# Kernel optimization log

Measured on AMD Instinct MI355X. Metric: run time of the kernel, lower is better.

## Reference

```python
import jax, jax.numpy as jnp
import numpy as np

B, N, D = 4, 4096, 1024
H, F = 16, 256
HD = D // H
EPS_ATTN = 1e-8
EPS_LN = 1e-5


def setup_inputs() -> dict:
    key = jax.random.key(0)
    ks = jax.random.split(key, 10)
    def kaiming(k, shape):
        fan_in = shape[1]
        return jax.random.normal(k, shape, jnp.float32) * jnp.sqrt(2.0 / fan_in)
    # orthogonal-ish random projection (plain gaussian init, then QR per head)
    pm = jax.random.normal(ks[0], (H, HD, F), jnp.float32)
    return {
        "x": jax.random.normal(ks[1], (B, N, D), jnp.float32),
        "proj": pm,
        "w_qkv": kaiming(ks[2], (3 * D, D)),
        "w_out": kaiming(ks[3], (D, D)),
        "b_out": jnp.zeros((D,), jnp.float32),
        "gamma": jnp.ones((D,), jnp.float32),
        "beta": jnp.zeros((D,), jnp.float32),
        "w1": kaiming(ks[4], (4 * D, D)),
        "b1": jnp.zeros((4 * D,), jnp.float32),
        "w2": kaiming(ks[5], (D, 4 * D)),
        "b2": jnp.zeros((D,), jnp.float32),
    }


def _layernorm(x, gamma, beta):
    mu = jnp.mean(x, axis=-1, keepdims=True)
    var = jnp.var(x, axis=-1, keepdims=True)
    return (x - mu) * jax.lax.rsqrt(var + EPS_LN) * gamma + beta


def reference(x, proj, w_qkv, w_out, b_out, gamma, beta, w1, b1, w2, b2):
    residual = x
    b, n, d = x.shape
    qkv = x @ w_qkv.T                      # (b,n,3d)
    q, k, v = jnp.split(qkv, 3, axis=-1)
    def to_heads(t):
        return t.reshape(b, n, H, HD).transpose(0, 2, 1, 3)  # (b,h,n,hd)
    q, k, v = to_heads(q), to_heads(k), to_heads(v)
    # kernel feature maps: elu(x)+1
    q_f = jax.nn.elu(jnp.einsum('bhnd,hdf->bhnf', q, proj)) + 1.0
    k_f = jax.nn.elu(jnp.einsum('bhnd,hdf->bhnf', k, proj)) + 1.0
    # non-causal FAVOR+ linear attention
    kv = jnp.einsum('bhnf,bhnd->bhfd', k_f, v)               # (b,h,f,hd)
    attn = jnp.einsum('bhnf,bhfd->bhnd', q_f, kv)            # (b,h,n,hd)
    k_sum = jnp.sum(k_f, axis=2)                             # (b,h,f)
    z = 1.0 / (jnp.einsum('bhnf,bhf->bhn', q_f, k_sum) + EPS_ATTN)
    attn = attn * z[..., None]
    attn = attn.transpose(0, 2, 1, 3).reshape(b, n, d)
    x = residual + attn @ w_out.T + b_out
    x = _layernorm(x, gamma, beta)
    h = jax.nn.gelu(x @ w1.T + b1, approximate=False)
    x = x + h @ w2.T + b2
    x = _layernorm(x, gamma, beta)
    return x
```

## Files before the change

kernel.cpp:

```cpp
#include <hip/hip_runtime.h>
#include <math.h>

typedef unsigned short u16;
typedef __bf16 bf16x8 __attribute__((ext_vector_type(8)));
typedef float f32x4 __attribute__((ext_vector_type(4)));
typedef unsigned short u16x4 __attribute__((ext_vector_type(4)));
typedef unsigned short u16x8 __attribute__((ext_vector_type(8)));

#define DEV static __device__ __forceinline__

DEV float bf2f(u16 u) { union { unsigned int i; float f; } x; x.i = ((unsigned int)u) << 16; return x.f; }
DEV u16 f2bf(float f) { union { float f; unsigned int i; } x; x.f = f; unsigned int r = x.i + 0x7fffu + ((x.i >> 16) & 1u); return (u16)(r >> 16); }

DEV void load_lds16(const void* g, void* l) {
  __builtin_amdgcn_global_load_lds((__attribute__((address_space(1))) void*)g,
                                   (__attribute__((address_space(3))) void*)l, 16, 0, 0);
}

#define MMAQ(AREG, BREG, MH, NH)                                                            \
  do {                                                                                      \
    __builtin_amdgcn_s_setprio(1);                                                          \
    _Pragma("unroll") for (int m_ = 0; m_ < 4; ++m_)                                        \
      _Pragma("unroll") for (int n_ = 0; n_ < 2; ++n_)                                      \
        _Pragma("unroll") for (int kk_ = 0; kk_ < 2; ++kk_)                                 \
          acc[(MH)*4 + m_][(NH)*2 + n_] = __builtin_amdgcn_mfma_f32_16x16x32_bf16(          \
              AREG[m_][kk_], BREG[n_][kk_], acc[(MH)*4 + m_][(NH)*2 + n_], 0, 0, 0);        \
    __builtin_amdgcn_s_setprio(0);                                                          \
  } while (0)

template<int EPI>
__global__ __launch_bounds__(512, 1)
void gemm256(const u16* __restrict__ A, const u16* __restrict__ B, void* __restrict__ Cv,
             const float* __restrict__ aux0, const float* __restrict__ aux1,
             int M, int N, int K, int lda, int ldb, int ldc)
{
  __shared__ __align__(16) unsigned char smem[131072];
  const int tid = threadIdx.x;
  int bx = blockIdx.x, by = blockIdx.y;
  {
    int nwg = gridDim.x * gridDim.y;
    if ((nwg & 7) == 0) {
      int wg = by * gridDim.x + bx;
      int swz = (wg & 7) * (nwg >> 3) + (wg >> 3);
      bx = swz % gridDim.x; by = swz / gridDim.x;
    }
  }
  const int m0 = by * 256, n0 = bx * 256;
  const int wid = tid >> 6, lane = tid & 63;
  const int wr = wid >> 2, wc = wid & 3;
  const int ln15 = lane & 15, lq = lane >> 4;
  const int bhalf = wc >> 1;
  const int sRow = tid >> 3, sCh = tid & 7;

  f32x4 acc[8][4] = {};
  bf16x8 aR[4][2], b0R[2][2], b1R[2][2];

  auto stageHalf = [&](const u16* G, int ld, int grs, int k0, int ldsoff) {
#pragma unroll
    for (int i = 0; i < 2; ++i) {
      int row = i * 64 + sRow;
      const unsigned char* src = (const unsigned char*)(G + (size_t)(grs + row) * ld + k0)
                               + ((sCh ^ (row & 7)) << 4);
      load_lds16(src, smem + ldsoff + row * 128 + sCh * 16);
    }
  };
  auto stageTile = [&](int k0, int dbuf) {
    stageHalf(A, lda, m0,       k0, (dbuf * 2 + 0) * 16384);
    stageHalf(A, lda, m0 + 128, k0, (dbuf * 2 + 1) * 16384);
    stageHalf(B, ldb, n0,       k0, 65536 + (dbuf * 2 + 0) * 16384);
    stageHalf(B, ldb, n0 + 128, k0, 65536 + (dbuf * 2 + 1) * 16384);
  };
  auto loadA = [&](int cur, int mh) {
    const unsigned char* base = smem + (cur * 2 + wr) * 16384;
#pragma unroll
    for (int m = 0; m < 4; ++m) {
      int rl = (mh * 4 + m) * 16 + ln15;
#pragma unroll
      for (int kk = 0; kk < 2; ++kk)
        aR[m][kk] = *(const bf16x8*)(base + rl * 128 + (((kk * 4 + lq) ^ (rl & 7)) << 4));
    }
  };
  auto loadB = [&](int cur, int nh, bf16x8 (&bq)[2][2]) {
    const unsigned char* base = smem + 65536 + (cur * 2 + bhalf) * 16384;
#pragma unroll
    for (int n = 0; n < 2; ++n) {
      int rb = (wc & 1) * 64 + (nh * 2 + n) * 16 + ln15;
#pragma unroll
      for (int kk = 0; kk < 2; ++kk)
        bq[n][kk] = *(const bf16x8*)(base + rb * 128 + (((kk * 4 + lq) ^ (rb & 7)) << 4));
    }
  };

  const int nkt = K >> 6;

  stageTile(0, 0);
  asm volatile("s_waitcnt vmcnt(0)" ::: "memory");
  __builtin_amdgcn_s_barrier();

  for (int t = 0; t < nkt; ++t) {
    const int cur = t & 1;
    const bool pf = (t + 1 < nkt);
    loadA(cur, 0);
    loadB(cur, 0, b0R);
    if (pf) stageTile((t + 1) << 6, cur ^ 1);
    __builtin_amdgcn_s_barrier();
    MMAQ(aR, b0R, 0, 0);
    __builtin_amdgcn_s_barrier();
    loadB(cur, 1, b1R);
    __builtin_amdgcn_s_barrier();
    MMAQ(aR, b1R, 0, 1);
    __builtin_amdgcn_s_barrier();
    loadA(cur, 1);
    __builtin_amdgcn_s_barrier();
    MMAQ(aR, b0R, 1, 0);
    __builtin_amdgcn_s_barrier();
    MMAQ(aR, b1R, 1, 1);
    if (pf) { asm volatile("s_waitcnt vmcnt(0)" ::: "memory"); }
    __builtin_amdgcn_s_barrier();
  }

#pragma unroll
  for (int m = 0; m < 8; ++m) {
#pragma unroll
    for (int n = 0; n < 4; ++n) {
      int col = n0 + wc * 64 + n * 16 + ln15;
#pragma unroll
      for (int j = 0; j < 4; ++j) {
        int row = m0 + wr * 128 + m * 16 + lq * 4 + j;
        float v = acc[m][n][j];
        size_t idx = (size_t)row * ldc + col;
        if (EPI == 0) {
          ((u16*)Cv)[idx] = f2bf(v);
        } else if (EPI == 3) {
          ((float*)Cv)[idx] = v + aux0[col] + aux1[idx];
        } else if (EPI == 4) {
          float g = v + aux0[col];
          float o = 0.5f * g * (1.f + erff(g * 0.70710678118f));
          ((u16*)Cv)[idx] = f2bf(o);
        }
      }
    }
  }
}

__global__ __launch_bounds__(256, 2)
void fused_kv(const u16* __restrict__ qkv, const u16* __restrict__ projT,
              float* __restrict__ kvpart, float* __restrict__ ksumpart)
{
  __shared__ __align__(16) unsigned char ktS[2][8192];
  __shared__ __align__(16) unsigned char vtS[2][8192];
  __shared__ __align__(16) unsigned char kfS[32768];
  const int tid = threadIdx.x;
  const int bh = blockIdx.y, chunk = blockIdx.x;
  const int b = bh >> 4, h = bh & 15;
  const int wid = tid >> 6, lane = tid & 63;
  const int ln15 = lane & 15, lq = lane >> 4;
  const int vN = tid >> 2, vD = (tid & 3) * 16;
  const int vCn = vN >> 3, vWb = (vN & 7) * 2;

  bf16x8 pf[4][2];
#pragma unroll
  for (int m = 0; m < 4; ++m)
#pragma unroll
    for (int kk = 0; kk < 2; ++kk) {
      int f = wid * 64 + m * 16 + ln15;
      pf[m][kk] = *(const bf16x8*)(projT + (size_t)h * 16384 + (size_t)f * 64 + (kk * 4 + lq) * 8);
    }

  float ksum_r = 0.f;
  f32x4 acc2[4][4] = {};
  const int nbase = chunk * 512;

  {
    const u16* kg = qkv + ((size_t)b * 4096 + nbase) * 3072 + 1024 + h * 64;
#pragma unroll
    for (int i = 0; i < 2; ++i) {
      int c = i * 256 + tid; int r = c >> 3, ch = c & 7;
      load_lds16((const unsigned char*)(kg + (size_t)r * 3072) + ((ch ^ (r & 7)) << 4),
                 ktS[0] + r * 128 + ch * 16);
    }
    const u16* vg = qkv + ((size_t)b * 4096 + nbase + vN) * 3072 + 2048 + h * 64 + vD;
    u16x8 va = *(const u16x8*)vg;
    u16x8 vb = *(const u16x8*)(vg + 8);
#pragma unroll
    for (int j = 0; j < 8; ++j) {
      int d = vD + j;
      *(u16*)(vtS[0] + d * 128 + ((vCn ^ (d & 7)) << 4) + vWb) = va[j];
    }
#pragma unroll
    for (int j = 0; j < 8; ++j) {
      int d = vD + 8 + j;
      *(u16*)(vtS[0] + d * 128 + ((vCn ^ (d & 7)) << 4) + vWb) = vb[j];
    }
  }
  __syncthreads();

  for (int t = 0; t < 8; ++t) {
    const int cur = t & 1, nxt = cur ^ 1;
    u16x8 va, vb;
    const bool havenext = (t + 1 < 8);
    if (havenext) {
      int n1 = nbase + (t + 1) * 64;
      const u16* kg = qkv + ((size_t)b * 4096 + n1) * 3072 + 1024 + h * 64;
#pragma unroll
      for (int i = 0; i < 2; ++i) {
        int c = i * 256 + tid; int r = c >> 3, ch = c & 7;
        load_lds16((const unsigned char*)(kg + (size_t)r * 3072) + ((ch ^ (r & 7)) << 4),
                   ktS[nxt] + r * 128 + ch * 16);
      }
      const u16* vg = qkv + ((size_t)b * 4096 + n1 + vN) * 3072 + 2048 + h * 64 + vD;
      va = *(const u16x8*)vg;
      vb = *(const u16x8*)(vg + 8);
    }

    bf16x8 bvk[2][4];
#pragma unroll
    for (int kk = 0; kk < 2; ++kk)
#pragma unroll
      for (int n = 0; n < 4; ++n) {
        int r = n * 16 + ln15, kc = kk * 4 + lq;
        bvk[kk][n] = *(const bf16x8*)(ktS[cur] + r * 128 + ((kc ^ (r & 7)) << 4));
      }
#pragma unroll
    for (int m = 0; m < 4; ++m) {
      f32x4 a1[4] = {};
#pragma unroll
      for (int kk = 0; kk < 2; ++kk)
#pragma unroll
        for (int n = 0; n < 4; ++n)
          a1[n] = __builtin_amdgcn_mfma_f32_16x16x32_bf16(pf[m][kk], bvk[kk][n], a1[n], 0, 0, 0);
#pragma unroll
      for (int n = 0; n < 4; ++n) {
        int nloc = n * 16 + ln15;
        int c = nloc >> 3, wb = (nloc & 7) * 2;
#pragma unroll
        for (int j = 0; j < 4; ++j) {
          int f = wid * 64 + m * 16 + lq * 4 + j;
          float v = a1[n][j];
          float o = v > 0.f ? v + 1.f : __expf(v);
          *(u16*)(kfS + f * 128 + ((c ^ (f & 7)) << 4) + wb) = f2bf(o);
        }
      }
    }
    __syncthreads();

    {
      int f = tid;
      float s = 0.f;
#pragma unroll
      for (int c = 0; c < 8; ++c) {
        u16x8 v = *(const u16x8*)(kfS + f * 128 + ((c ^ (f & 7)) << 4));
#pragma unroll
        for (int j = 0; j < 8; ++j) s += bf2f(v[j]);
      }
      ksum_r += s;
    }
#pragma unroll
    for (int kk = 0; kk < 2; ++kk) {
      int kc = kk * 4 + lq;
      bf16x8 af[4], bv[4];
#pragma unroll
      for (int m = 0; m < 4; ++m) { int r = wid * 64 + m * 16 + ln15; af[m] = *(const bf16x8*)(kfS + r * 128 + ((kc ^ (r & 7)) << 4)); }
#pragma unroll
      for (int n = 0; n < 4; ++n) { int r = n * 16 + ln15; bv[n] = *(const bf16x8*)(vtS[cur] + r * 128 + ((kc ^ (r & 7)) << 4)); }
#pragma unroll
      for (int m = 0; m < 4; ++m)
#pragma unroll
        for (int n = 0; n < 4; ++n)
          acc2[m][n] = __builtin_amdgcn_mfma_f32_16x16x32_bf16(af[m], bv[n], acc2[m][n], 0, 0, 0);
    }
    if (havenext) {
#pragma unroll
      for (int j = 0; j < 8; ++j) {
        int d = vD + j;
        *(u16*)(vtS[nxt] + d * 128 + ((vCn ^ (d & 7)) << 4) + vWb) = va[j];
      }
#pragma unroll
      for (int j = 0; j < 8; ++j) {
        int d = vD + 8 + j;
        *(u16*)(vtS[nxt] + d * 128 + ((vCn ^ (d & 7)) << 4) + vWb) = vb[j];
      }
    }
    __syncthreads();
  }

  const size_t pbase = ((size_t)bh * 8 + chunk) * 16384;
#pragma unroll
  for (int half = 0; half < 2; ++half) {
#pragma unroll
    for (int m = 0; m < 4; ++m)
#pragma unroll
      for (int n2 = 0; n2 < 2; ++n2) {
        int n = half * 2 + n2;
        int dloc = n2 * 16 + ln15;
        int f = wid * 64 + m * 16 + lq * 4;
        *(f32x4*)(kfS + dloc * 1024 + ((f * 4) ^ ((dloc & 7) << 4))) = acc2[m][n];
      }
    __syncthreads();
#pragma unroll
    for (int k = 0; k < 8; ++k) {
      int dloc = k * 4 + wid;
      f32x4 val = *(const f32x4*)(kfS + dloc * 1024 + ((lane * 16) ^ ((dloc & 7) << 4)));
      *(f32x4*)(kvpart + pbase + (size_t)(half * 32 + dloc) * 256 + lane * 4) = val;
    }
    __syncthreads();
  }
  ksumpart[((size_t)bh * 8 + chunk) * 256 + tid] = ksum_r;
}

__global__ __launch_bounds__(256) void kv_finalize(const float* __restrict__ kvpart,
    const float* __restrict__ ksumpart, u16* __restrict__ kvT, float* __restrict__ ksum)
{
  int bx = blockIdx.x, bh = bx >> 2, dq = bx & 3, tid = threadIdx.x;
  const float* base = kvpart + (size_t)bh * 131072;
  u16* out = kvT + (size_t)bh * 16384;
#pragma unroll
  for (int k = 0; k < 16; ++k) {
    int idx = dq * 4096 + k * 256 + tid;
    float s = 0.f;
#pragma unroll
    for (int c = 0; c < 8; ++c) s += base[(size_t)c * 16384 + idx];
    out[idx] = f2bf(s);
  }
  if (dq == 0) {
    float s = 0.f;
#pragma unroll
    for (int c = 0; c < 8; ++c) s += ksumpart[((size_t)bh * 8 + c) * 256 + tid];
    ksum[(size_t)bh * 256 + tid] = s;
  }
}

__global__ __launch_bounds__(256, 3)
void fused_attn(const u16* __restrict__ qkv, const u16* __restrict__ projT,
                const u16* __restrict__ kvT, const float* __restrict__ ksum,
                u16* __restrict__ attnb)
{
  __shared__ __align__(16) unsigned char qtS[8192];
  __shared__ __align__(16) unsigned char qfS[32768];
  __shared__ float zpart[64][4];
  __shared__ float zS[64];
  const int tid = threadIdx.x;
  const int bh = blockIdx.y, nt = blockIdx.x;
  const int b = bh >> 4, h = bh & 15;
  const int wid = tid >> 6, lane = tid & 63;
  const int ln15 = lane & 15, lq = lane >> 4;
  const int n0 = nt * 64;

  bf16x8 pf[4][2];
#pragma unroll
  for (int n = 0; n < 4; ++n)
#pragma unroll
    for (int kk = 0; kk < 2; ++kk) {
      int f = wid * 64 + n * 16 + ln15;
      pf[n][kk] = *(const bf16x8*)(projT + (size_t)h * 16384 + (size_t)f * 64 + (kk * 4 + lq) * 8);
    }

  const u16* qg = qkv + ((size_t)b * 4096 + n0) * 3072 + h * 64;
#pragma unroll
  for (int i = 0; i < 2; ++i) {
    int c = i * 256 + tid; int r = c >> 3, ch = c & 7;
    load_lds16((const unsigned char*)(qg + (size_t)r * 3072) + ((ch ^ (r & 7)) << 4),
               qtS + r * 128 + ch * 16);
  }
  __syncthreads();

#pragma unroll
  for (int m = 0; m < 4; ++m) {
    bf16x8 af[2];
#pragma unroll
    for (int kk = 0; kk < 2; ++kk) {
      int r = m * 16 + ln15, kc = kk * 4 + lq;
      af[kk] = *(const bf16x8*)(qtS + r * 128 + ((kc ^ (r & 7)) << 4));
    }
    f32x4 a1[4] = {};
#pragma unroll
    for (int kk = 0; kk < 2; ++kk)
#pragma unroll
      for (int n = 0; n < 4; ++n)
        a1[n] = __builtin_amdgcn_mfma_f32_16x16x32_bf16(af[kk], pf[n][kk], a1[n], 0, 0, 0);
#pragma unroll
    for (int n = 0; n < 4; ++n) {
      int f = wid * 64 + n * 16 + ln15;
      int c = f >> 3, wb = (f & 7) * 2;
#pragma unroll
      for (int j = 0; j < 4; ++j) {
        int row = m * 16 + lq * 4 + j;
        float v = a1[n][j];
        float o = v > 0.f ? v + 1.f : __expf(v);
        *(u16*)(qfS + row * 512 + ((c ^ (row & 7)) << 4) + wb) = f2bf(o);
      }
    }
  }
  __syncthreads();

  {
    int n = tid & 63, q = tid >> 6;
    const float* kp = ksum + (size_t)bh * 256;
    float s = 0.f;
#pragma unroll
    for (int c = q * 8; c < q * 8 + 8; ++c) {
      u16x8 v = *(const u16x8*)(qfS + n * 512 + ((c ^ (n & 7)) << 4));
#pragma unroll
      for (int j = 0; j < 8; ++j) s += bf2f(v[j]) * kp[c * 8 + j];
    }
    zpart[n][q] = s;
  }
  __syncthreads();
  if (tid < 64) zS[tid] = 1.f / (zpart[tid][0] + zpart[tid][1] + zpart[tid][2] + zpart[tid][3] + 1e-8f);
  __syncthreads();

  f32x4 a2[4] = {};
  const u16* kvg = kvT + (size_t)bh * 16384;
#pragma unroll
  for (int kk = 0; kk < 8; ++kk) {
    int kc = kk * 4 + lq;
    int r = wid * 16 + ln15;
    bf16x8 af = *(const bf16x8*)(qfS + r * 512 + ((kc ^ (r & 7)) << 4));
#pragma unroll
    for (int nf = 0; nf < 4; ++nf) {
      int d = nf * 16 + ln15;
      bf16x8 bv = *(const bf16x8*)(kvg + (size_t)d * 256 + kc * 8);
      a2[nf] = __builtin_amdgcn_mfma_f32_16x16x32_bf16(af, bv, a2[nf], 0, 0, 0);
    }
  }
#pragma unroll
  for (int nf = 0; nf < 4; ++nf)
#pragma unroll
    for (int j = 0; j < 4; ++j) {
      int d = nf * 16 + ln15;
      int n = wid * 16 + lq * 4 + j;
      float v = a2[nf][j] * zS[n];
      attnb[((size_t)b * 4096 + n0 + n) * 1024 + h * 64 + d] = f2bf(v);
    }
}

__global__ __launch_bounds__(256) void cast_kernel(const float* __restrict__ in, u16* __restrict__ out, int n4)
{
  int i = blockIdx.x * 256 + threadIdx.x;
  if (i >= n4) return;
  float4 v = ((const float4*)in)[i];
  u16x4 o = { f2bf(v.x), f2bf(v.y), f2bf(v.z), f2bf(v.w) };
  ((u16x4*)out)[i] = o;
}

__global__ __launch_bounds__(256) void projt_kernel(const float* __restrict__ proj, u16* __restrict__ out)
{
  int i = blockIdx.x * 256 + threadIdx.x;
  int d = i & 63, f = (i >> 6) & 255, h = i >> 14;
  out[i] = f2bf(proj[((size_t)h * 64 + d) * 256 + f]);
}

__global__ __launch_bounds__(256) void ln_kernel(const float* __restrict__ in, const float* __restrict__ gamma,
                                                 const float* __restrict__ beta, float* __restrict__ outF,
                                                 u16* __restrict__ outB)
{
  int row = blockIdx.x, tid = threadIdx.x;
  float4 v = ((const float4*)(in + (size_t)row * 1024))[tid];
  float s = v.x + v.y + v.z + v.w;
  float q = v.x * v.x + v.y * v.y + v.z * v.z + v.w * v.w;
  for (int off = 32; off; off >>= 1) { s += __shfl_down(s, off); q += __shfl_down(q, off); }
  __shared__ float rs[4], rq[4];
  int wid = tid >> 6, lane = tid & 63;
  if (!lane) { rs[wid] = s; rq[wid] = q; }
  __syncthreads();
  s = rs[0] + rs[1] + rs[2] + rs[3];
  q = rq[0] + rq[1] + rq[2] + rq[3];
  float mu = s * (1.f / 1024.f);
  float rstd = rsqrtf(q * (1.f / 1024.f) - mu * mu + 1e-5f);
  float4 g = ((const float4*)gamma)[tid];
  float4 bb = ((const float4*)beta)[tid];
  float4 o;
  o.x = (v.x - mu) * rstd * g.x + bb.x;
  o.y = (v.y - mu) * rstd * g.y + bb.y;
  o.z = (v.z - mu) * rstd * g.z + bb.z;
  o.w = (v.w - mu) * rstd * g.w + bb.w;
  ((float4*)(outF + (size_t)row * 1024))[tid] = o;
  if (outB) {
    u16x4 ob = { f2bf(o.x), f2bf(o.y), f2bf(o.z), f2bf(o.w) };
    ((u16x4*)(outB + (size_t)row * 1024))[tid] = ob;
  }
}

#define O_WQKVB   0L
#define O_WOUTB   6291456L
#define O_W1B     8388608L
#define O_W2B     16777216L
#define O_PROJT   25165824L
#define O_KSUM    25690112L
#define O_KSP     26804224L
#define O_KVB     27852800L
#define O_QFG     37289984L
#define O_QKVB    70844416L
#define O_ATTNB   171507712L
#define WS_NEED   205062144L

extern "C" void kernel_launch(void* const* d_in, const int* in_sizes, int n_in,
                              void* d_out, int out_size, void* d_ws, size_t ws_size,
                              hipStream_t stream)
{
  if (ws_size < (size_t)WS_NEED) return;

  const float* x     = (const float*)d_in[0];
  const float* proj  = (const float*)d_in[1];
  const float* wqkv  = (const float*)d_in[2];
  const float* wout  = (const float*)d_in[3];
  const float* bout  = (const float*)d_in[4];
  const float* gamma = (const float*)d_in[5];
  const float* beta  = (const float*)d_in[6];
  const float* w1    = (const float*)d_in[7];
  const float* b1    = (const float*)d_in[8];
  const float* w2    = (const float*)d_in[9];
  const float* b2    = (const float*)d_in[10];
  float* outp = (float*)d_out;
  char* ws = (char*)d_ws;

  u16* wqkvb  = (u16*)(ws + O_WQKVB);
  u16* woutb  = (u16*)(ws + O_WOUTB);
  u16* w1b    = (u16*)(ws + O_W1B);
  u16* w2b    = (u16*)(ws + O_W2B);
  u16* projTb = (u16*)(ws + O_PROJT);
  float* ksumf= (float*)(ws + O_KSUM);
  float* ksp  = (float*)(ws + O_KSP);
  u16* kvTb   = (u16*)(ws + O_KVB);
  u16* qkvb   = (u16*)(ws + O_QKVB);
  u16* attnb  = (u16*)(ws + O_ATTNB);
  u16* x1b    = (u16*)(ws + O_QFG);
  u16* hfull  = (u16*)(ws + O_QKVB);

  u16* xbD   = (u16*)d_out;
  float* kvp = (float*)d_out;

  cast_kernel<<<16384, 256, 0, stream>>>(x, xbD, 4194304);
  cast_kernel<<<3072, 256, 0, stream>>>(wqkv, wqkvb, 786432);
  cast_kernel<<<1024, 256, 0, stream>>>(wout, woutb, 262144);
  cast_kernel<<<4096, 256, 0, stream>>>(w1, w1b, 1048576);
  cast_kernel<<<4096, 256, 0, stream>>>(w2, w2b, 1048576);
  projt_kernel<<<1024, 256, 0, stream>>>(proj, projTb);

  gemm256<0><<<dim3(12, 64), 512, 0, stream>>>(xbD, wqkvb, qkvb, nullptr, nullptr,
      16384, 3072, 1024, 1024, 1024, 3072);

  fused_kv<<<dim3(8, 64), 256, 0, stream>>>(qkvb, projTb, kvp, ksp);
  kv_finalize<<<256, 256, 0, stream>>>(kvp, ksp, kvTb, ksumf);
  fused_attn<<<dim3(64, 64), 256, 0, stream>>>(qkvb, projTb, kvTb, ksumf, attnb);

  gemm256<3><<<dim3(4, 64), 512, 0, stream>>>(attnb, woutb, outp, bout, x,
      16384, 1024, 1024, 1024, 1024, 1024);

  ln_kernel<<<16384, 256, 0, stream>>>(outp, gamma, beta, outp, x1b);

  gemm256<4><<<dim3(16, 64), 512, 0, stream>>>(x1b, w1b, hfull, b1, nullptr,
      16384, 4096, 1024, 1024, 1024, 4096);

  gemm256<3><<<dim3(4, 64), 512, 0, stream>>>(hfull, w2b, outp, b2, outp,
      16384, 1024, 4096, 4096, 4096, 1024);

  ln_kernel<<<16384, 256, 0, stream>>>(outp, gamma, beta, outp, nullptr);
}
```

Measured before the change: 737.2 us.

## Prefetch GEMM tiles two iterations ahead and precompute LDS/global addresses

The main GEMM loop used to issue the next tile's global-to-LDS load at the start of each iteration and wait for it at the end. It now primes two tiles up front. It stages tile t+2 into the buffer that was just consumed, after the last LDS reads of the iteration, and uses a partial vmcnt wait so one tile's loads stay in flight. Global source pointers and LDS read/write offsets are precomputed once, then advanced or XOR-toggled instead of being recomputed each iteration. The aim is to hide more global-load latency and cut address arithmetic, at the cost of more live registers and tighter reliance on correct waitcnt accounting.

```diff
diff --git a/kernel.cpp b/kernel.cpp
--- a/kernel.cpp
+++ b/kernel.cpp
@@ -2,6 +2,7 @@
 #include <math.h>
 
 typedef unsigned short u16;
+typedef unsigned char u8;
 typedef __bf16 bf16x8 __attribute__((ext_vector_type(8)));
 typedef float f32x4 __attribute__((ext_vector_type(4)));
 typedef unsigned short u16x4 __attribute__((ext_vector_type(4)));
@@ -55,68 +56,79 @@
   f32x4 acc[8][4] = {};
   bf16x8 aR[4][2], b0R[2][2], b1R[2][2];
 
-  auto stageHalf = [&](const u16* G, int ld, int grs, int k0, int ldsoff) {
-#pragma unroll
-    for (int i = 0; i < 2; ++i) {
-      int row = i * 64 + sRow;
-      const unsigned char* src = (const unsigned char*)(G + (size_t)(grs + row) * ld + k0)
-                               + ((sCh ^ (row & 7)) << 4);
-      load_lds16(src, smem + ldsoff + row * 128 + sCh * 16);
-    }
-  };
-  auto stageTile = [&](int k0, int dbuf) {
-    stageHalf(A, lda, m0,       k0, (dbuf * 2 + 0) * 16384);
-    stageHalf(A, lda, m0 + 128, k0, (dbuf * 2 + 1) * 16384);
-    stageHalf(B, ldb, n0,       k0, 65536 + (dbuf * 2 + 0) * 16384);
-    stageHalf(B, ldb, n0 + 128, k0, 65536 + (dbuf * 2 + 1) * 16384);
-  };
-  auto loadA = [&](int cur, int mh) {
-    const unsigned char* base = smem + (cur * 2 + wr) * 16384;
-#pragma unroll
-    for (int m = 0; m < 4; ++m) {
-      int rl = (mh * 4 + m) * 16 + ln15;
-#pragma unroll
-      for (int kk = 0; kk < 2; ++kk)
-        aR[m][kk] = *(const bf16x8*)(base + rl * 128 + (((kk * 4 + lq) ^ (rl & 7)) << 4));
-    }
-  };
-  auto loadB = [&](int cur, int nh, bf16x8 (&bq)[2][2]) {
-    const unsigned char* base = smem + 65536 + (cur * 2 + bhalf) * 16384;
-#pragma unroll
-    for (int n = 0; n < 2; ++n) {
-      int rb = (wc & 1) * 64 + (nh * 2 + n) * 16 + ln15;
-#pragma unroll
-      for (int kk = 0; kk < 2; ++kk)
-        bq[n][kk] = *(const bf16x8*)(base + rb * 128 + (((kk * 4 + lq) ^ (rb & 7)) << 4));
-    }
-  };
+  const u8* gsrc[8];
+  unsigned ldst[8];
+  {
+    const int r0 = sRow, r1 = sRow + 64;
+    const unsigned sc0 = (unsigned)((sCh ^ (r0 & 7)) << 4);
+    const unsigned sc1 = (unsigned)((sCh ^ (r1 & 7)) << 4);
+    gsrc[0] = (const u8*)(A + (size_t)(m0 + r0) * lda) + sc0;
+    gsrc[1] = (const u8*)(A + (size_t)(m0 + r1) * lda) + sc1;
+    gsrc[2] = (const u8*)(A + (size_t)(m0 + 128 + r0) * lda) + sc0;
+    gsrc[3] = (const u8*)(A + (size_t)(m0 + 128 + r1) * lda) + sc1;
+    gsrc[4] = (const u8*)(B + (size_t)(n0 + r0) * ldb) + sc0;
+    gsrc[5] = (const u8*)(B + (size_t)(n0 + r1) * ldb) + sc1;
+    gsrc[6] = (const u8*)(B + (size_t)(n0 + 128 + r0) * ldb) + sc0;
+    gsrc[7] = (const u8*)(B + (size_t)(n0 + 128 + r1) * ldb) + sc1;
+    const unsigned base = (unsigned)(sRow * 128 + sCh * 16);
+    ldst[0] = base;            ldst[1] = base + 8192;
+    ldst[2] = base + 16384;    ldst[3] = base + 16384 + 8192;
+    ldst[4] = base + 65536;    ldst[5] = base + 65536 + 8192;
+    ldst[6] = base + 81920;    ldst[7] = base + 81920 + 8192;
+  }
+#define STAGE(BUFSEL)                                                      \
+  do {                                                                     \
+    const unsigned bo_ = (unsigned)(BUFSEL) << 15;                         \
+    _Pragma("unroll") for (int j_ = 0; j_ < 8; ++j_)                       \
+      load_lds16(gsrc[j_], smem + (ldst[j_] + bo_));                       \
+  } while (0)
+#define ADV()                                                              \
+  do { _Pragma("unroll") for (int j_ = 0; j_ < 8; ++j_) gsrc[j_] += 128; } while (0)
+
+  const unsigned swk0 = (unsigned)(((0 * 4 + lq) ^ (ln15 & 7)) << 4);
+  const unsigned swk1 = (unsigned)(((1 * 4 + lq) ^ (ln15 & 7)) << 4);
+  unsigned aOff0 = (unsigned)(wr * 16384 + ln15 * 128) + swk0;
+  unsigned aOff1 = (unsigned)(wr * 16384 + ln15 * 128) + swk1;
+  unsigned bOff0 = (unsigned)(65536 + bhalf * 16384 + ((wc & 1) * 64 + ln15) * 128) + swk0;
+  unsigned bOff1 = (unsigned)(65536 + bhalf * 16384 + ((wc & 1) * 64 + ln15) * 128) + swk1;
+#define LDA(MH)                                                                     \
+  do { _Pragma("unroll") for (int m_ = 0; m_ < 4; ++m_) {                           \
+    aR[m_][0] = *(const bf16x8*)(smem + aOff0 + ((MH) * 8192 + m_ * 2048));         \
+    aR[m_][1] = *(const bf16x8*)(smem + aOff1 + ((MH) * 8192 + m_ * 2048));         \
+  } } while (0)
+#define LDB(NH, BQ)                                                                 \
+  do { _Pragma("unroll") for (int n_ = 0; n_ < 2; ++n_) {                           \
+    BQ[n_][0] = *(const bf16x8*)(smem + bOff0 + ((NH) * 4096 + n_ * 2048));         \
+    BQ[n_][1] = *(const bf16x8*)(smem + bOff1 + ((NH) * 4096 + n_ * 2048));         \
+  } } while (0)
 
   const int nkt = K >> 6;
 
-  stageTile(0, 0);
-  asm volatile("s_waitcnt vmcnt(0)" ::: "memory");
+  STAGE(0); ADV();
+  STAGE(1); ADV();
+  asm volatile("s_waitcnt vmcnt(8)" ::: "memory");
   __builtin_amdgcn_s_barrier();
 
   for (int t = 0; t < nkt; ++t) {
-    const int cur = t & 1;
-    const bool pf = (t + 1 < nkt);
-    loadA(cur, 0);
-    loadB(cur, 0, b0R);
-    if (pf) stageTile((t + 1) << 6, cur ^ 1);
+    LDA(0); LDB(0, b0R);
     __builtin_amdgcn_s_barrier();
     MMAQ(aR, b0R, 0, 0);
     __builtin_amdgcn_s_barrier();
-    loadB(cur, 1, b1R);
+    LDB(1, b1R);
     __builtin_amdgcn_s_barrier();
     MMAQ(aR, b1R, 0, 1);
     __builtin_amdgcn_s_barrier();
-    loadA(cur, 1);
+    LDA(1);
     __builtin_amdgcn_s_barrier();
     MMAQ(aR, b0R, 1, 0);
     __builtin_amdgcn_s_barrier();
+    const bool pf2 = (t + 2 < nkt);
+    if (pf2) { STAGE(t & 1); ADV(); }
     MMAQ(aR, b1R, 1, 1);
-    if (pf) { asm volatile("s_waitcnt vmcnt(0)" ::: "memory"); }
-    __builtin_amdgcn_s_barrier();
+    if (pf2) asm volatile("s_waitcnt vmcnt(8)" ::: "memory");
+    else     asm volatile("s_waitcnt vmcnt(0)" ::: "memory");
+    __builtin_amdgcn_s_barrier();
+    aOff0 ^= 32768; aOff1 ^= 32768; bOff0 ^= 32768; bOff1 ^= 32768;
   }
 
 #pragma unroll
@@ -141,6 +153,10 @@
       }
     }
   }
+#undef STAGE
+#undef ADV
+#undef LDA
+#undef LDB
 }
 
 __global__ __launch_bounds__(256, 2)
```

New measurement: 724.3 us. No clear change (-1.8%).
